# Kernel optimization log

Hardware: AMD Instinct MI355X
Metric: run time of the kernel (lower is better)

## Reference

```python
import jax, jax.numpy as jnp
import numpy as np
import math

B, P, PIX, D, C = 128, 256, 256, 512, 10
MAX_STEPS, TOL, EPS = 4, 1e-3, 1e-5


def setup_inputs() -> dict:
    key = jax.random.key(0)
    ks = jax.random.split(key, 12)
    pi = math.pi
    return {
        "x": jax.random.normal(ks[0], (B, P, PIX), jnp.float32),
        "Wp": jax.random.normal(ks[1], (D, PIX), jnp.float32) * (1.0 / math.sqrt(PIX)),
        "bp": jnp.zeros((D,), jnp.float32),
        "q_rot": jax.random.uniform(ks[2], (D,), jnp.float32, -pi, pi),
        "k_rot": jax.random.uniform(ks[3], (D,), jnp.float32, -pi, pi),
        "v_rot": jax.random.uniform(ks[4], (D,), jnp.float32, -pi, pi),
        "ff_real": jax.random.normal(ks[5], (D, D), jnp.float32) * (1.0 / math.sqrt(D)),
        "ff_imag": jax.random.uniform(ks[6], (D, D), jnp.float32, -0.01, 0.01),
        "Wr": jax.random.normal(ks[7], (C, D), jnp.float32) * 0.05,
        "br": jnp.zeros((C,), jnp.float32),
        "Wi": jax.random.normal(ks[8], (C, D), jnp.float32) * 0.05,
        "bi": jnp.zeros((C,), jnp.float32),
    }


def _complex_norm(x):
    # normalize magnitude stats over last dim, preserve phase (torch.std uses ddof=1)
    mag = jnp.abs(x)
    mean_mag = jnp.mean(mag, axis=-1, keepdims=True)
    std_mag = jnp.std(mag, axis=-1, keepdims=True, ddof=1)
    norm_mag = (mag - mean_mag) / (std_mag + EPS)
    scale = jnp.tanh(norm_mag) / (mag + EPS)
    return x * scale


def _fro(z):
    return jnp.sqrt(jnp.sum(jnp.abs(z) ** 2))


def _pos_phase():
    pos = jnp.arange(P, dtype=jnp.float32)[:, None]
    dim = jnp.arange(D, dtype=jnp.float32)[None, :]
    freq = 1.0 / (10000.0 ** (dim / D))
    return pos * freq * math.pi  # (P, D)


def reference(x, Wp, bp, q_rot, k_rot, v_rot, ff_real, ff_imag, Wr, br, Wi, bi):
    mag = jnp.tanh(jnp.einsum('bpi,di->bpd', x, Wp) + bp)
    state = mag.astype(jnp.complex64) * jnp.exp(1j * _pos_phase())[None]  # (B,P,D)
    ff = (ff_real + 1j * ff_imag).astype(jnp.complex64)
    eq, ek, ev = jnp.exp(1j * q_rot), jnp.exp(1j * k_rot), jnp.exp(1j * v_rot)
    scale = 8.0 / math.sqrt(D)
    active = jnp.array(True)
    for _ in range(MAX_STEPS):  # fixed small iteration count; updates frozen after convergence
        prev = state
        q, k, v = state * eq, state * ek, state * ev
        interference = jnp.einsum('bpd,bqd->bpq', q, jnp.conj(k))
        attn = jax.nn.softmax(interference.real * scale, axis=-1)
        attn_out = jnp.einsum('bpq,bqd->bpd', attn.astype(jnp.complex64), v)
        new_state = _complex_norm((prev + attn_out) @ ff)
        diff = _fro(new_state - prev) / (_fro(new_state) + 1e-8)
        state = jnp.where(active, new_state, prev)
        active = jnp.logical_and(active, diff >= TOL)
    pooled = jnp.mean(state, axis=1)  # (B,D) complex
    logits = pooled.real @ Wr.T + br + pooled.imag @ Wi.T + bi
    return logits
```

## Files before the change

kernel.cpp:

```cpp
#include <hip/hip_runtime.h>
#include <math.h>

#define BB   128
#define PP   256
#define PIX_ 256
#define DD   512
#define CC   10
#define MTOT (BB*PP)
#define NK   1024
#define KA   2048
#define KB2  2048
#define NSLOT (MTOT/4)

static constexpr float SCALE_F = 0.35355339059327373f;
static constexpr float PI_F    = 3.14159265358979323846f;

typedef short bf16x8 __attribute__((ext_vector_type(8)));
typedef float f32x4  __attribute__((ext_vector_type(4)));

__device__ __forceinline__ unsigned short f2bf(float f) {
    union { float f; unsigned u; } v; v.f = f;
    unsigned r = v.u + 0x7FFF + ((v.u >> 16) & 1);
    return (unsigned short)(r >> 16);
}
__device__ __forceinline__ float bf2f(unsigned short h) {
    union { unsigned u; float f; } v; v.u = ((unsigned)h) << 16;
    return v.f;
}

typedef __attribute__((address_space(3))) unsigned lds_u32;
typedef __attribute__((address_space(1))) const unsigned glb_u32;
__device__ __forceinline__ void gl2lds16(const unsigned short* g, short* l) {
    __builtin_amdgcn_global_load_lds((glb_u32*)g, (lds_u32*)l, 16, 0, 0);
}

__global__ void k_setup(const float* __restrict__ q_rot, const float* __restrict__ k_rot,
                        const float* __restrict__ v_rot,
                        float* __restrict__ freq, float* __restrict__ cd, float* __restrict__ sd,
                        float* __restrict__ cv, float* __restrict__ sv,
                        int* __restrict__ active) {
    int t = threadIdx.x;
    if (t < DD) {
        freq[t] = expf(-(float)t * (9.210340371976184f / 512.0f));
        float dl = q_rot[t] - k_rot[t];
        cd[t] = cosf(dl);       sd[t] = sinf(dl);
        cv[t] = cosf(v_rot[t]); sv[t] = sinf(v_rot[t]);
    }
    if (t == 0) *active = 1;
}

__global__ __launch_bounds__(256) void k_prep2(const float* __restrict__ Fr, const float* __restrict__ Fi,
                                               unsigned short* __restrict__ Bt2) {
    const int n = blockIdx.x;
    const int t = threadIdx.x;
    unsigned short* row = Bt2 + (size_t)n * KB2;
#pragma unroll
    for (int j4 = 0; j4 < 4; j4++) {
        const int j = j4 * 256 + t;
        float v;
        if (n < 512) v = (j < 512) ? Fr[(size_t)j * DD + n] : -Fi[(size_t)(j - 512) * DD + n];
        else         v = (j < 512) ? Fi[(size_t)j * DD + (n - 512)] : Fr[(size_t)(j - 512) * DD + (n - 512)];
        const unsigned short hi = f2bf(v);
        row[j] = hi;
        row[NK + j] = f2bf(v - bf2f(hi));
    }
}

__global__ __launch_bounds__(256) void k_packx(const float* __restrict__ x, unsigned short* __restrict__ Xp) {
    const int r = blockIdx.x, t = threadIdx.x;
    const float v = x[(size_t)r * PIX_ + t];
    const unsigned short h = f2bf(v);
    Xp[(size_t)r * 512 + t] = h;
    Xp[(size_t)r * 512 + 256 + t] = f2bf(v - bf2f(h));
}

__global__ __launch_bounds__(256) void k_wpack(const float* __restrict__ Wp, unsigned short* __restrict__ Wt) {
    const int d = blockIdx.x, t = threadIdx.x;
    const float v = Wp[(size_t)d * PIX_ + t];
    const unsigned short h = f2bf(v);
    Wt[(size_t)d * 512 + t] = h;
    Wt[(size_t)d * 512 + 256 + t] = f2bf(v - bf2f(h));
}

#define SCAT4(TILE, V4) do { TILE[lk+0][lrow]=(V4).x; TILE[lk+1][lrow]=(V4).y; \
                             TILE[lk+2][lrow]=(V4).z; TILE[lk+3][lrow]=(V4).w; } while(0)

__global__ __launch_bounds__(256) void k_init(const float* __restrict__ x,
        const float* __restrict__ Wp, const float* __restrict__ bp,
        const float* __restrict__ freq,
        float* __restrict__ Sr, float* __restrict__ Si) {
    __shared__ float As[16][68];
    __shared__ float Bs[16][68];
    const int bm = blockIdx.y * 64, bn = blockIdx.x * 64;
    const int t = threadIdx.x, tx = t & 15, ty = t >> 4;
    const int lrow = t >> 2, lk = (t & 3) * 4;
    float acc[4][4] = {};
    for (int k0 = 0; k0 < PIX_; k0 += 16) {
        const float4 a4 = *(const float4*)(x  + (size_t)(bm + lrow) * PIX_ + k0 + lk);
        const float4 b4 = *(const float4*)(Wp + (size_t)(bn + lrow) * PIX_ + k0 + lk);
        __syncthreads();
        SCAT4(As, a4);
        SCAT4(Bs, b4);
        __syncthreads();
#pragma unroll
        for (int kk = 0; kk < 16; ++kk) {
            const float4 av = *(const float4*)&As[kk][ty * 4];
            const float4 bv = *(const float4*)&Bs[kk][tx * 4];
            const float a[4] = {av.x, av.y, av.z, av.w};
            const float b[4] = {bv.x, bv.y, bv.z, bv.w};
#pragma unroll
            for (int i = 0; i < 4; i++)
#pragma unroll
                for (int j = 0; j < 4; j++) acc[i][j] = fmaf(a[i], b[j], acc[i][j]);
        }
    }
#pragma unroll
    for (int i = 0; i < 4; i++) {
        const int m = bm + ty * 4 + i;
        const int p = m & 255;
        float4 vr, vi;
        float* pvr = (float*)&vr; float* pvi = (float*)&vi;
#pragma unroll
        for (int j = 0; j < 4; j++) {
            const int d = bn + tx * 4 + j;
            const float mg = tanhf(acc[i][j] + bp[d]);
            const float ph = (float)p * freq[d] * PI_F;
            float sph, cph; sincosf(ph, &sph, &cph);
            pvr[j] = mg * cph; pvi[j] = mg * sph;
        }
        *(float4*)(Sr + (size_t)m * DD + bn + tx * 4) = vr;
        *(float4*)(Si + (size_t)m * DD + bn + tx * 4) = vi;
    }
}

__global__ __launch_bounds__(256) void k_init_mfma(const unsigned short* __restrict__ Xp,
        const unsigned short* __restrict__ Wt, const float* __restrict__ bp,
        const float* __restrict__ freq,
        float* __restrict__ Sr, float* __restrict__ Si) {
    __shared__ short AH[128][32], AL[128][32];
    __shared__ short BH[128][32], BL[128][32];
    const int t = threadIdx.x, w = t >> 6, L = t & 63;
    const int lane15 = L & 15, quad = L >> 4;
    const int bm = blockIdx.y * 128, bn = blockIdx.x * 128;
    const int gr = t >> 2, ch = (t & 3) * 8;
    short* AHw = &AH[0][0] + w * 512;
    short* ALw = &AL[0][0] + w * 512;
    short* BHw = &BH[0][0] + w * 512;
    short* BLw = &BL[0][0] + w * 512;
    f32x4 acc[2][8] = {};
    for (int k0 = 0; k0 < 256; k0 += 32) {
        __syncthreads();
        gl2lds16(Xp + (size_t)(bm + gr) * 512      + k0 + ch,       AHw);
        gl2lds16(Xp + (size_t)(bm + 64 + gr) * 512 + k0 + ch,       AHw + 64 * 32);
        gl2lds16(Xp + (size_t)(bm + gr) * 512      + 256 + k0 + ch, ALw);
        gl2lds16(Xp + (size_t)(bm + 64 + gr) * 512 + 256 + k0 + ch, ALw + 64 * 32);
        gl2lds16(Wt + (size_t)(bn + gr) * 512      + k0 + ch,       BHw);
        gl2lds16(Wt + (size_t)(bn + 64 + gr) * 512 + k0 + ch,       BHw + 64 * 32);
        gl2lds16(Wt + (size_t)(bn + gr) * 512      + 256 + k0 + ch, BLw);
        gl2lds16(Wt + (size_t)(bn + 64 + gr) * 512 + 256 + k0 + ch, BLw + 64 * 32);
        __syncthreads();
        bf16x8 ah[2], al[2];
#pragma unroll
        for (int tr = 0; tr < 2; tr++) {
            ah[tr] = *(const bf16x8*)&AH[w * 32 + tr * 16 + lane15][quad * 8];
            al[tr] = *(const bf16x8*)&AL[w * 32 + tr * 16 + lane15][quad * 8];
        }
#pragma unroll
        for (int tc = 0; tc < 8; tc++) {
            const bf16x8 bh = *(const bf16x8*)&BH[tc * 16 + lane15][quad * 8];
            acc[0][tc] = __builtin_amdgcn_mfma_f32_16x16x32_bf16(ah[0], bh, acc[0][tc], 0, 0, 0);
            acc[1][tc] = __builtin_amdgcn_mfma_f32_16x16x32_bf16(ah[1], bh, acc[1][tc], 0, 0, 0);
            acc[0][tc] = __builtin_amdgcn_mfma_f32_16x16x32_bf16(al[0], bh, acc[0][tc], 0, 0, 0);
            acc[1][tc] = __builtin_amdgcn_mfma_f32_16x16x32_bf16(al[1], bh, acc[1][tc], 0, 0, 0);
            const bf16x8 bl = *(const bf16x8*)&BL[tc * 16 + lane15][quad * 8];
            acc[0][tc] = __builtin_amdgcn_mfma_f32_16x16x32_bf16(ah[0], bl, acc[0][tc], 0, 0, 0);
            acc[1][tc] = __builtin_amdgcn_mfma_f32_16x16x32_bf16(ah[1], bl, acc[1][tc], 0, 0, 0);
        }
    }
#pragma unroll
    for (int tr = 0; tr < 2; tr++)
#pragma unroll
        for (int tc = 0; tc < 8; tc++) {
            const int d = bn + tc * 16 + lane15;
            const float bpd = bp[d];
            const float fq = freq[d] * PI_F;
#pragma unroll
            for (int r = 0; r < 4; r++) {
                const int m = bm + w * 32 + tr * 16 + quad * 4 + r;
                const int p = m & 255;
                const float mg = tanhf(acc[tr][tc][r] + bpd);
                float sph, cph; sincosf((float)p * fq, &sph, &cph);
                Sr[(size_t)m * DD + d] = mg * cph;
                Si[(size_t)m * DD + d] = mg * sph;
            }
        }
}

__global__ __launch_bounds__(256) void k_xy(const float* __restrict__ Sr, const float* __restrict__ Si,
        const float* __restrict__ cd, const float* __restrict__ sd,
        unsigned short* X, unsigned short* Y,
        const int* __restrict__ active) {
    if (*active == 0) return;
    const int r = blockIdx.x, t = threadIdx.x;
    const size_t base = (size_t)r * DD + 2 * t;
    const float2 s_r = *(const float2*)(Sr + base);
    const float2 s_i = *(const float2*)(Si + base);
    const float2 c2  = *(const float2*)(cd + 2 * t);
    const float2 s2  = *(const float2*)(sd + 2 * t);
    unsigned short* xr = X + (size_t)r * KA;
    unsigned short* yr = Y + (size_t)r * KA;
    const float srv[2] = {s_r.x, s_r.y}, siv[2] = {s_i.x, s_i.y};
    const float cv_[2] = {c2.x, c2.y},  sv_[2] = {s2.x, s2.y};
    ushort2 xh_r, xh_i, xl_r, xl_i, yh_r, yh_i, yl_r, yl_i;
    unsigned short* o[8] = {(unsigned short*)&xh_r, (unsigned short*)&xh_i,
                            (unsigned short*)&xl_r, (unsigned short*)&xl_i,
                            (unsigned short*)&yh_r, (unsigned short*)&yh_i,
                            (unsigned short*)&yl_r, (unsigned short*)&yl_i};
#pragma unroll
    for (int e = 0; e < 2; e++) {
        const unsigned short hr = f2bf(srv[e]);
        const unsigned short hi_ = f2bf(siv[e]);
        o[0][e] = hr;  o[2][e] = f2bf(srv[e] - bf2f(hr));
        o[1][e] = hi_; o[3][e] = f2bf(siv[e] - bf2f(hi_));
        const float krr = srv[e] * cv_[e] + siv[e] * sv_[e];
        const float kri = siv[e] * cv_[e] - srv[e] * sv_[e];
        const unsigned short yh1 = f2bf(krr);
        const unsigned short yh2 = f2bf(kri);
        o[4][e] = yh1; o[6][e] = f2bf(krr - bf2f(yh1));
        o[5][e] = yh2; o[7][e] = f2bf(kri - bf2f(yh2));
    }
    *(ushort2*)(xr + 2 * t)        = xh_r;
    *(ushort2*)(xr + 512 + 2 * t)  = xh_i;
    *(ushort2*)(xr + 1024 + 2 * t) = xl_r;
    *(ushort2*)(xr + 1536 + 2 * t) = xl_i;
    *(ushort2*)(yr + 2 * t)        = yh_r;
    *(ushort2*)(yr + 512 + 2 * t)  = yh_i;
    *(ushort2*)(yr + 1024 + 2 * t) = yl_r;
    *(ushort2*)(yr + 1536 + 2 * t) = yl_i;
}

__global__ __launch_bounds__(256) void k_score_sm(const unsigned short* __restrict__ X,
        const unsigned short* __restrict__ Y,
        unsigned short* __restrict__ Asp, const int* __restrict__ active) {
    if (*active == 0) return;
    __shared__ short XH[64][32], XL[64][32];
    __shared__ short YH[256][32], YL[256][32];
    const int t = threadIdx.x;
    const int w = t >> 6, L = t & 63;
    const int lane15 = L & 15, quad = L >> 4;
    const int bm = blockIdx.x * 64;
    const int yb = ((int)blockIdx.x >> 2) * 256;
    const int gr = t >> 2, ch = (t & 3) * 8;
    short* XHw = &XH[0][0] + w * 512;
    short* XLw = &XL[0][0] + w * 512;
    short* YHw = &YH[0][0] + w * 512;
    short* YLw = &YL[0][0] + w * 512;
    f32x4 acc[16] = {};
    for (int k0 = 0; k0 < 1024; k0 += 32) {
        __syncthreads();
        gl2lds16(X + (size_t)(bm + gr) * KA + k0 + ch,        XHw);
        gl2lds16(X + (size_t)(bm + gr) * KA + 1024 + k0 + ch, XLw);
#pragma unroll
        for (int s = 0; s < 4; s++) {
            gl2lds16(Y + (size_t)(yb + s * 64 + gr) * KA + k0 + ch,        YHw + s * 2048);
            gl2lds16(Y + (size_t)(yb + s * 64 + gr) * KA + 1024 + k0 + ch, YLw + s * 2048);
        }
        __syncthreads();
        const bf16x8 xh = *(const bf16x8*)&XH[w * 16 + lane15][quad * 8];
        const bf16x8 xl = *(const bf16x8*)&XL[w * 16 + lane15][quad * 8];
#pragma unroll
        for (int tc = 0; tc < 16; tc++) {
            const bf16x8 yh = *(const bf16x8*)&YH[tc * 16 + lane15][quad * 8];
            acc[tc] = __builtin_amdgcn_mfma_f32_16x16x32_bf16(xh, yh, acc[tc], 0, 0, 0);
            acc[tc] = __builtin_amdgcn_mfma_f32_16x16x32_bf16(xl, yh, acc[tc], 0, 0, 0);
            const bf16x8 yl = *(const bf16x8*)&YL[tc * 16 + lane15][quad * 8];
            acc[tc] = __builtin_amdgcn_mfma_f32_16x16x32_bf16(xh, yl, acc[tc], 0, 0, 0);
        }
    }
#pragma unroll
    for (int tc = 0; tc < 16; tc++) acc[tc] *= SCALE_F;
#pragma unroll
    for (int r = 0; r < 4; r++) {
        float mx = acc[0][r];
#pragma unroll
        for (int tc = 1; tc < 16; tc++) mx = fmaxf(mx, acc[tc][r]);
#pragma unroll
        for (int off = 8; off; off >>= 1) mx = fmaxf(mx, __shfl_xor(mx, off, 64));
        float s = 0.f;
        float e[16];
#pragma unroll
        for (int tc = 0; tc < 16; tc++) { e[tc] = __expf(acc[tc][r] - mx); s += e[tc]; }
#pragma unroll
        for (int off = 8; off; off >>= 1) s += __shfl_xor(s, off, 64);
        const float inv = 1.0f / s;
        const int row = bm + w * 16 + quad * 4 + r;
        unsigned short* o = Asp + (size_t)row * 512;
#pragma unroll
        for (int tc = 0; tc < 16; tc++) {
            const float p = e[tc] * inv;
            const unsigned short h = f2bf(p);
            o[tc * 16 + lane15] = h;
            o[256 + tc * 16 + lane15] = f2bf(p - bf2f(h));
        }
    }
}

__global__ __launch_bounds__(256) void k_attnout_mfma(const unsigned short* __restrict__ Asp,
        const unsigned short* __restrict__ X,
        const float* __restrict__ Sr, const float* __restrict__ Si,
        const float* __restrict__ cv, const float* __restrict__ sv,
        unsigned short* __restrict__ A2, const int* __restrict__ active) {
    if (*active == 0) return;
    __shared__ short AhT[128][32];
    __shared__ short AlT[128][32];
    __shared__ short BH[128][40];
    __shared__ short BL[128][40];
    const int t = threadIdx.x;
    const int w = t >> 6, L = t & 63;
    const int lane15 = L & 15, quad = L >> 4;
    const int bm = blockIdx.y * 128;
    const int bn = blockIdx.x * 64;
    const int sample = blockIdx.y >> 1;
    const int gr = t >> 2, ch = (t & 3) * 8;
    short* AhW0 = &AhT[0][0] + w * 512;
    short* AhW1 = AhW0 + 64 * 32;
    short* AlW0 = &AlT[0][0] + w * 512;
    short* AlW1 = AlW0 + 64 * 32;
    const int nn = t & 127, kh = t >> 7;
    const unsigned short* Bsrc = X + (size_t)sample * PP * KA
                               + ((nn < 64) ? (bn + nn) : (512 + bn + nn - 64));
    f32x4 acc[2][8] = {};
    for (int q0 = 0; q0 < PP; q0 += 32) {
        __syncthreads();
        gl2lds16(Asp + (size_t)(bm + gr) * 512      + q0 + ch,       AhW0);
        gl2lds16(Asp + (size_t)(bm + 64 + gr) * 512 + q0 + ch,       AhW1);
        gl2lds16(Asp + (size_t)(bm + gr) * 512      + 256 + q0 + ch, AlW0);
        gl2lds16(Asp + (size_t)(bm + 64 + gr) * 512 + 256 + q0 + ch, AlW1);
#pragma unroll
        for (int kg = 0; kg < 2; kg++) {
            const int qb = kh * 16 + kg * 8;
            bf16x8 hh, ll;
#pragma unroll
            for (int j = 0; j < 8; j++) {
                const size_t o = (size_t)(q0 + qb + j) * KA;
                hh[j] = (short)Bsrc[o];
                ll[j] = (short)Bsrc[o + 1024];
            }
            *(bf16x8*)&BH[nn][qb] = hh;
            *(bf16x8*)&BL[nn][qb] = ll;
        }
        __syncthreads();
        bf16x8 bh[8];
#pragma unroll
        for (int tc = 0; tc < 8; tc++)
            bh[tc] = *(const bf16x8*)&BH[tc * 16 + lane15][quad * 8];
        bf16x8 afh[2];
#pragma unroll
        for (int tr = 0; tr < 2; tr++) {
            afh[tr] = *(const bf16x8*)&AhT[w * 32 + tr * 16 + lane15][quad * 8];
            const bf16x8 afl = *(const bf16x8*)&AlT[w * 32 + tr * 16 + lane15][quad * 8];
#pragma unroll
            for (int tc = 0; tc < 8; tc++)
                acc[tr][tc] = __builtin_amdgcn_mfma_f32_16x16x32_bf16(afh[tr], bh[tc], acc[tr][tc], 0, 0, 0);
#pragma unroll
            for (int tc = 0; tc < 8; tc++)
                acc[tr][tc] = __builtin_amdgcn_mfma_f32_16x16x32_bf16(afl, bh[tc], acc[tr][tc], 0, 0, 0);
        }
#pragma unroll
        for (int tc = 0; tc < 8; tc++) {
            const bf16x8 bl = *(const bf16x8*)&BL[tc * 16 + lane15][quad * 8];
            acc[0][tc] = __builtin_amdgcn_mfma_f32_16x16x32_bf16(afh[0], bl, acc[0][tc], 0, 0, 0);
            acc[1][tc] = __builtin_amdgcn_mfma_f32_16x16x32_bf16(afh[1], bl, acc[1][tc], 0, 0, 0);
        }
    }
#pragma unroll
    for (int tr = 0; tr < 2; tr++) {
#pragma unroll
        for (int tc = 0; tc < 4; tc++) {
            const int d = bn + tc * 16 + lane15;
            const float cvd = cv[d], svd = sv[d];
#pragma unroll
            for (int r = 0; r < 4; r++) {
                const int m = bm + w * 32 + tr * 16 + quad * 4 + r;
                const float wr = acc[tr][tc][r];
                const float wi = acc[tr][tc + 4][r];
                const float tr_ = Sr[(size_t)m * DD + d] + (wr * cvd - wi * svd);
                const float ti_ = Si[(size_t)m * DD + d] + (wr * svd + wi * cvd);
                const unsigned short rh = f2bf(tr_);
                const unsigned short ih = f2bf(ti_);
                unsigned short* arow = A2 + (size_t)m * KA;
                arow[d]        = rh;
                arow[512 + d]  = ih;
                arow[1024 + d] = f2bf(tr_ - bf2f(rh));
                arow[1536 + d] = f2bf(ti_ - bf2f(ih));
            }
        }
    }
}

__global__ __launch_bounds__(256) void k_ff_mfma2(const unsigned short* __restrict__ A2,
        const unsigned short* __restrict__ Bt2,
        float* __restrict__ U, const int* __restrict__ active) {
    if (*active == 0) return;
    __shared__ short AH[128][32], AL[128][32];
    __shared__ short BH[128][32], BL[128][32];
    const int t = threadIdx.x;
    const int w = t >> 6, L = t & 63;
    const int lane15 = L & 15, quad = L >> 4;
    const int bm = blockIdx.y * 128, bn = blockIdx.x * 128;
    const int gr = t >> 2, ch = (t & 3) * 8;
    short* AHw = &AH[0][0] + w * 512;
    short* ALw = &AL[0][0] + w * 512;
    short* BHw = &BH[0][0] + w * 512;
    short* BLw = &BL[0][0] + w * 512;
    f32x4 acc[2][8] = {};
    for (int k0 = 0; k0 < 1024; k0 += 32) {
        __syncthreads();
        gl2lds16(A2  + (size_t)(bm + gr) * KA       + k0 + ch,        AHw);
        gl2lds16(A2  + (size_t)(bm + 64 + gr) * KA  + k0 + ch,        AHw + 64 * 32);
        gl2lds16(A2  + (size_t)(bm + gr) * KA       + 1024 + k0 + ch, ALw);
        gl2lds16(A2  + (size_t)(bm + 64 + gr) * KA  + 1024 + k0 + ch, ALw + 64 * 32);
        gl2lds16(Bt2 + (size_t)(bn + gr) * KB2      + k0 + ch,        BHw);
        gl2lds16(Bt2 + (size_t)(bn + 64 + gr) * KB2 + k0 + ch,        BHw + 64 * 32);
        gl2lds16(Bt2 + (size_t)(bn + gr) * KB2      + 1024 + k0 + ch, BLw);
        gl2lds16(Bt2 + (size_t)(bn + 64 + gr) * KB2 + 1024 + k0 + ch, BLw + 64 * 32);
        __syncthreads();
        bf16x8 ah[2], al[2];
#pragma unroll
        for (int tr = 0; tr < 2; tr++) {
            ah[tr] = *(const bf16x8*)&AH[w * 32 + tr * 16 + lane15][quad * 8];
            al[tr] = *(const bf16x8*)&AL[w * 32 + tr * 16 + lane15][quad * 8];
        }
#pragma unroll
        for (int tc = 0; tc < 8; tc++) {
            const bf16x8 bh = *(const bf16x8*)&BH[tc * 16 + lane15][quad * 8];
            acc[0][tc] = __builtin_amdgcn_mfma_f32_16x16x32_bf16(ah[0], bh, acc[0][tc], 0, 0, 0);
            acc[1][tc] = __builtin_amdgcn_mfma_f32_16x16x32_bf16(ah[1], bh, acc[1][tc], 0, 0, 0);
            acc[0][tc] = __builtin_amdgcn_mfma_f32_16x16x32_bf16(al[0], bh, acc[0][tc], 0, 0, 0);
            acc[1][tc] = __builtin_amdgcn_mfma_f32_16x16x32_bf16(al[1], bh, acc[1][tc], 0, 0, 0);
            const bf16x8 bl = *(const bf16x8*)&BL[tc * 16 + lane15][quad * 8];
            acc[0][tc] = __builtin_amdgcn_mfma_f32_16x16x32_bf16(ah[0], bl, acc[0][tc], 0, 0, 0);
            acc[1][tc] = __builtin_amdgcn_mfma_f32_16x16x32_bf16(ah[1], bl, acc[1][tc], 0, 0, 0);
        }
    }
#pragma unroll
    for (int tr = 0; tr < 2; tr++)
#pragma unroll
        for (int tc = 0; tc < 8; tc++) {
            const int n = bn + tc * 16 + lane15;
            const int mbase = bm + w * 32 + tr * 16 + quad * 4;
#pragma unroll
            for (int r = 0; r < 4; r++)
                U[(size_t)(mbase + r) * NK + n] = acc[tr][tc][r];
        }
}

__global__ __launch_bounds__(256) void k_norm(const float* U,
        float* __restrict__ Sr, float* __restrict__ Si,
        float* __restrict__ part,
        unsigned short* X, unsigned short* Y,
        const float* __restrict__ cd, const float* __restrict__ sd,
        const int wxy, const int* __restrict__ active) {
    if (*active == 0) return;
    __shared__ float red[8];
    const int t = threadIdx.x, rt = t >> 6, L = t & 63;
    const int row = blockIdx.x * 4 + rt;
    const size_t ub = (size_t)row * NK;
    const size_t base = (size_t)row * DD;
    const float4 ur0 = *(const float4*)(U + ub + 4 * L);
    const float4 ur1 = *(const float4*)(U + ub + 256 + 4 * L);
    const float4 ui0 = *(const float4*)(U + ub + 512 + 4 * L);
    const float4 ui1 = *(const float4*)(U + ub + 768 + 4 * L);
    const float4 pr0 = *(const float4*)(Sr + base + 4 * L);
    const float4 pr1 = *(const float4*)(Sr + base + 256 + 4 * L);
    const float4 pi0 = *(const float4*)(Si + base + 4 * L);
    const float4 pi1 = *(const float4*)(Si + base + 256 + 4 * L);
    const float urr[8] = {ur0.x, ur0.y, ur0.z, ur0.w, ur1.x, ur1.y, ur1.z, ur1.w};
    const float uii[8] = {ui0.x, ui0.y, ui0.z, ui0.w, ui1.x, ui1.y, ui1.z, ui1.w};
    float mg[8], msum = 0.f;
#pragma unroll
    for (int e = 0; e < 8; e++) {
        mg[e] = sqrtf(urr[e] * urr[e] + uii[e] * uii[e]);
        msum += mg[e];
    }
#pragma unroll
    for (int off = 32; off; off >>= 1) msum += __shfl_xor(msum, off, 64);
    const float mean = msum * (1.0f / 512.0f);
    float vs = 0.f;
#pragma unroll
    for (int e = 0; e < 8; e++) { const float d = mg[e] - mean; vs += d * d; }
#pragma unroll
    for (int off = 32; off; off >>= 1) vs += __shfl_xor(vs, off, 64);
    const float istd = 1.0f / (sqrtf(vs * (1.0f / 511.0f)) + 1e-5f);
    float nr[8], ni[8];
#pragma unroll
    for (int e = 0; e < 8; e++) {
        const float sc = tanhf((mg[e] - mean) * istd) / (mg[e] + 1e-5f);
        nr[e] = urr[e] * sc; ni[e] = uii[e] * sc;
    }
    const float prr[8] = {pr0.x, pr0.y, pr0.z, pr0.w, pr1.x, pr1.y, pr1.z, pr1.w};
    const float pii[8] = {pi0.x, pi0.y, pi0.z, pi0.w, pi1.x, pi1.y, pi1.z, pi1.w};
    float dd = 0.f, nn = 0.f;
#pragma unroll
    for (int e = 0; e < 8; e++) {
        const float dr = nr[e] - prr[e], di = ni[e] - pii[e];
        dd += dr * dr + di * di;
        nn += nr[e] * nr[e] + ni[e] * ni[e];
    }
    *(float4*)(Sr + base + 4 * L)       = make_float4(nr[0], nr[1], nr[2], nr[3]);
    *(float4*)(Sr + base + 256 + 4 * L) = make_float4(nr[4], nr[5], nr[6], nr[7]);
    *(float4*)(Si + base + 4 * L)       = make_float4(ni[0], ni[1], ni[2], ni[3]);
    *(float4*)(Si + base + 256 + 4 * L) = make_float4(ni[4], ni[5], ni[6], ni[7]);
    if (wxy) {
        unsigned short* xr = X + (size_t)row * KA;
        unsigned short* yr = Y + (size_t)row * KA;
        const float4 c0 = *(const float4*)(cd + 4 * L);
        const float4 c1 = *(const float4*)(cd + 256 + 4 * L);
        const float4 s0 = *(const float4*)(sd + 4 * L);
        const float4 s1 = *(const float4*)(sd + 256 + 4 * L);
        const float cdv[8] = {c0.x, c0.y, c0.z, c0.w, c1.x, c1.y, c1.z, c1.w};
        const float sdv[8] = {s0.x, s0.y, s0.z, s0.w, s1.x, s1.y, s1.z, s1.w};
        ushort4 xhr[2], xhi[2], xlr[2], xli[2], yhr[2], yhi[2], ylr[2], yli[2];
#pragma unroll
        for (int e = 0; e < 8; e++) {
            const int g = e >> 2, j = e & 3;
            const unsigned short hr = f2bf(nr[e]);
            const unsigned short hi_ = f2bf(ni[e]);
            ((unsigned short*)&xhr[g])[j] = hr;
            ((unsigned short*)&xlr[g])[j] = f2bf(nr[e] - bf2f(hr));
            ((unsigned short*)&xhi[g])[j] = hi_;
            ((unsigned short*)&xli[g])[j] = f2bf(ni[e] - bf2f(hi_));
            const float krr = nr[e] * cdv[e] + ni[e] * sdv[e];
            const float kri = ni[e] * cdv[e] - nr[e] * sdv[e];
            const unsigned short k1 = f2bf(krr);
            const unsigned short k2 = f2bf(kri);
            ((unsigned short*)&yhr[g])[j] = k1;
            ((unsigned short*)&ylr[g])[j] = f2bf(krr - bf2f(k1));
            ((unsigned short*)&yhi[g])[j] = k2;
            ((unsigned short*)&yli[g])[j] = f2bf(kri - bf2f(k2));
        }
        *(ushort4*)(xr + 4 * L)        = xhr[0]; *(ushort4*)(xr + 256 + 4 * L)  = xhr[1];
        *(ushort4*)(xr + 512 + 4 * L)  = xhi[0]; *(ushort4*)(xr + 768 + 4 * L)  = xhi[1];
        *(ushort4*)(xr + 1024 + 4 * L) = xlr[0]; *(ushort4*)(xr + 1280 + 4 * L) = xlr[1];
        *(ushort4*)(xr + 1536 + 4 * L) = xli[0]; *(ushort4*)(xr + 1792 + 4 * L) = xli[1];
        *(ushort4*)(yr + 4 * L)        = yhr[0]; *(ushort4*)(yr + 256 + 4 * L)  = yhr[1];
        *(ushort4*)(yr + 512 + 4 * L)  = yhi[0]; *(ushort4*)(yr + 768 + 4 * L)  = yhi[1];
        *(ushort4*)(yr + 1024 + 4 * L) = ylr[0]; *(ushort4*)(yr + 1280 + 4 * L) = ylr[1];
        *(ushort4*)(yr + 1536 + 4 * L) = yli[0]; *(ushort4*)(yr + 1792 + 4 * L) = yli[1];
    }
#pragma unroll
    for (int off = 32; off; off >>= 1) {
        dd += __shfl_xor(dd, off, 64);
        nn += __shfl_xor(nn, off, 64);
    }
    if (L == 0) { red[rt] = dd; red[4 + rt] = nn; }
    __syncthreads();
    if (t == 0)
        *(float2*)(part + 2 * blockIdx.x) =
            make_float2(red[0] + red[1] + red[2] + red[3],
                        red[4] + red[5] + red[6] + red[7]);
}

__global__ __launch_bounds__(256) void k_flag(const float* __restrict__ part, int* __restrict__ active) {
    __shared__ float red[8];
    const int t = threadIdx.x, rt = t >> 6, L = t & 63;
    float dd = 0.f, nn = 0.f;
    for (int i = t; i < NSLOT; i += 256) {
        const float2 p = *(const float2*)(part + 2 * i);
        dd += p.x; nn += p.y;
    }
#pragma unroll
    for (int off = 32; off; off >>= 1) {
        dd += __shfl_xor(dd, off, 64);
        nn += __shfl_xor(nn, off, 64);
    }
    if (L == 0) { red[rt] = dd; red[4 + rt] = nn; }
    __syncthreads();
    if (t == 0) {
        const float d = red[0] + red[1] + red[2] + red[3];
        const float n = red[4] + red[5] + red[6] + red[7];
        const float diff = sqrtf(d) / (sqrtf(n) + 1e-8f);
        const int a = *active;
        *active = (a && (diff >= 1e-3f)) ? 1 : 0;
    }
}

__global__ __launch_bounds__(256) void k_pool(const float* __restrict__ Sr, const float* __restrict__ Si,
        float* __restrict__ Pr, float* __restrict__ Pi) {
    const int gid = blockIdx.x * 256 + threadIdx.x;
    const int b = gid >> 9, d = gid & 511;
    const size_t base = (size_t)b * PP * DD + d;
    float sr = 0.f, si = 0.f;
    for (int p = 0; p < PP; p++) {
        sr += Sr[base + (size_t)p * DD];
        si += Si[base + (size_t)p * DD];
    }
    Pr[gid] = sr * (1.0f / 256.0f);
    Pi[gid] = si * (1.0f / 256.0f);
}

__global__ __launch_bounds__(64) void k_logits(const float* __restrict__ Pr, const float* __restrict__ Pi,
        const float* __restrict__ Wr, const float* __restrict__ br,
        const float* __restrict__ Wi, const float* __restrict__ bi,
        float* __restrict__ out) {
    const int b = blockIdx.x;
    const int lane = threadIdx.x;
    for (int c = 0; c < CC; c++) {
        float acc = 0.f;
#pragma unroll
        for (int k = 0; k < 8; k++) {
            const int d = lane + 64 * k;
            acc += Pr[b * DD + d] * Wr[c * DD + d] + Pi[b * DD + d] * Wi[c * DD + d];
        }
#pragma unroll
        for (int off = 32; off; off >>= 1) acc += __shfl_xor(acc, off, 64);
        if (lane == 0) out[b * CC + c] = acc + br[c] + bi[c];
    }
}

extern "C" void kernel_launch(void* const* d_in, const int* in_sizes, int n_in,
                              void* d_out, int out_size, void* d_ws, size_t ws_size,
                              hipStream_t stream) {
    const float* x     = (const float*)d_in[0];
    const float* Wp    = (const float*)d_in[1];
    const float* bp    = (const float*)d_in[2];
    const float* q_rot = (const float*)d_in[3];
    const float* k_rot = (const float*)d_in[4];
    const float* v_rot = (const float*)d_in[5];
    const float* ffr   = (const float*)d_in[6];
    const float* ffi   = (const float*)d_in[7];
    const float* Wr    = (const float*)d_in[8];
    const float* br    = (const float*)d_in[9];
    const float* Wi    = (const float*)d_in[10];
    const float* bi    = (const float*)d_in[11];
    float* out = (float*)d_out;

    float* ws = (float*)d_ws;
    const size_t plane = (size_t)MTOT * DD;
    const size_t sline = (size_t)PP * DD;

    float* freq = ws;
    float* cd   = freq + DD;
    float* sd   = cd + DD;
    float* cv   = sd + DD;
    float* sv   = cv + DD;
    int*   active = (int*)(sv + DD);
    float* Pr = ws + 4096;
    float* Pi = Pr + (size_t)BB * DD;
    float* part = Pi + (size_t)BB * DD;
    float* Sr = part + 2 * NSLOT;
    float* Si = Sr + plane;
    unsigned short* Bt2 = (unsigned short*)(Si + plane);
    unsigned short* Wt  = Bt2 + (size_t)NK * KB2;
    float* chunkbase = Si + plane + (size_t)NK * 3072 / 2;

    const size_t fixed_f = (4096 + 2 * (size_t)BB * DD + 2 * NSLOT) + 2 * plane + (size_t)NK * 3072 / 2;
    const size_t perC_f = (size_t)PP * NK * 2 + (size_t)PP * 256;

    int C = BB;
    while (C > 1 && (fixed_f + (size_t)C * perC_f) * 4ull > ws_size) C >>= 1;
    const int fullXY = (C == BB);
    const int mfmaInit = (C >= 32);

    float* U = chunkbase;
    unsigned short* X  = (unsigned short*)chunkbase;
    float* Yf = chunkbase + (size_t)C * PP * NK;
    unsigned short* Y  = (unsigned short*)Yf;
    unsigned short* A2 = Y;
    unsigned short* Asp = (unsigned short*)(Yf + (size_t)C * PP * NK);
    unsigned short* Xp = (unsigned short*)chunkbase;

    k_setup<<<1, 512, 0, stream>>>(q_rot, k_rot, v_rot, freq, cd, sd, cv, sv, active);
    k_prep2<<<NK, 256, 0, stream>>>(ffr, ffi, Bt2);
    if (mfmaInit) {
        k_packx<<<MTOT, 256, 0, stream>>>(x, Xp);
        k_wpack<<<DD, 256, 0, stream>>>(Wp, Wt);
        k_init_mfma<<<dim3(DD / 128, MTOT / 128), 256, 0, stream>>>(Xp, Wt, bp, freq, Sr, Si);
    } else {
        k_init<<<dim3(DD / 64, MTOT / 64), 256, 0, stream>>>(x, Wp, bp, freq, Sr, Si);
    }

    for (int it = 0; it < 4; ++it) {
        for (int c0 = 0; c0 < BB; c0 += C) {
            float* Sr_c = Sr + (size_t)c0 * sline;
            float* Si_c = Si + (size_t)c0 * sline;
            float* part_c = part + (size_t)c0 * (PP / 4) * 2;
            if (!fullXY || it == 0)
                k_xy<<<C * PP, 256, 0, stream>>>(Sr_c, Si_c, cd, sd, X, Y, active);
            k_score_sm<<<C * 4, 256, 0, stream>>>(X, Y, Asp, active);
            k_attnout_mfma<<<dim3(8, C * 2), 256, 0, stream>>>(Asp, X, Sr_c, Si_c, cv, sv, A2, active);
            k_ff_mfma2<<<dim3(NK / 128, C * 2), 256, 0, stream>>>(A2, Bt2, U, active);
            k_norm<<<C * (PP / 4), 256, 0, stream>>>(U, Sr_c, Si_c, part_c, X, Y, cd, sd, fullXY, active);
        }
        k_flag<<<1, 256, 0, stream>>>(part, active);
    }

    k_pool<<<BB * DD / 256, 256, 0, stream>>>(Sr, Si, Pr, Pi);
    k_logits<<<BB, 64, 0, stream>>>(Pr, Pi, Wr, br, Wi, bi, out);
}
```

Baseline: 3.268 ms.

## Reorder block grids so M tiles vary fastest and stage init epilogue through LDS

Swaps the grid dimensions of the init, attention-output and FF GEMMs so consecutive workgroups walk along M while sharing the same N tile. The score kernel's block index is remapped to interleave samples, which changes which blocks run concurrently and so cache locality and spread across XCDs. The init GEMM epilogue now writes results into LDS tiles and emits coalesced float4 global stores instead of scattered scalar stores. The extra 68 KB of shared memory in init lowers its occupancy, and the grid reordering may lose B-tile reuse in L2.

```diff
diff --git a/kernel.cpp b/kernel.cpp
--- a/kernel.cpp
+++ b/kernel.cpp
@@ -139,9 +139,11 @@
         float* __restrict__ Sr, float* __restrict__ Si) {
     __shared__ short AH[128][32], AL[128][32];
     __shared__ short BH[128][32], BL[128][32];
+    __shared__ float TBr[128][68];
+    __shared__ float TBi[128][68];
     const int t = threadIdx.x, w = t >> 6, L = t & 63;
     const int lane15 = L & 15, quad = L >> 4;
-    const int bm = blockIdx.y * 128, bn = blockIdx.x * 128;
+    const int bm = blockIdx.x * 128, bn = blockIdx.y * 128;
     const int gr = t >> 2, ch = (t & 3) * 8;
     short* AHw = &AH[0][0] + w * 512;
     short* ALw = &AL[0][0] + w * 512;
@@ -178,22 +180,37 @@
         }
     }
 #pragma unroll
-    for (int tr = 0; tr < 2; tr++)
-#pragma unroll
-        for (int tc = 0; tc < 8; tc++) {
-            const int d = bn + tc * 16 + lane15;
-            const float bpd = bp[d];
-            const float fq = freq[d] * PI_F;
-#pragma unroll
-            for (int r = 0; r < 4; r++) {
-                const int m = bm + w * 32 + tr * 16 + quad * 4 + r;
-                const int p = m & 255;
-                const float mg = tanhf(acc[tr][tc][r] + bpd);
-                float sph, cph; sincosf((float)p * fq, &sph, &cph);
-                Sr[(size_t)m * DD + d] = mg * cph;
-                Si[(size_t)m * DD + d] = mg * sph;
+    for (int h = 0; h < 2; h++) {
+        __syncthreads();
+#pragma unroll
+        for (int tr = 0; tr < 2; tr++)
+#pragma unroll
+            for (int tc = 0; tc < 4; tc++) {
+                const int tcg = h * 4 + tc;
+                const int d = bn + tcg * 16 + lane15;
+                const float bpd = bp[d];
+                const float fq = freq[d] * PI_F;
+#pragma unroll
+                for (int r = 0; r < 4; r++) {
+                    const int m = w * 32 + tr * 16 + quad * 4 + r;
+                    const int p = (bm + m) & 255;
+                    const float mg = tanhf(acc[tr][tcg][r] + bpd);
+                    float sph, cph; sincosf((float)p * fq, &sph, &cph);
+                    TBr[m][tc * 16 + lane15] = mg * cph;
+                    TBi[m][tc * 16 + lane15] = mg * sph;
+                }
             }
-        }
+        __syncthreads();
+#pragma unroll
+        for (int g = 0; g < 8; g++) {
+            const int row = (t >> 4) + g * 16;
+            const int col = (t & 15) * 4;
+            const float4 vr = *(const float4*)&TBr[row][col];
+            const float4 vi = *(const float4*)&TBi[row][col];
+            *(float4*)(Sr + (size_t)(bm + row) * DD + bn + h * 64 + col) = vr;
+            *(float4*)(Si + (size_t)(bm + row) * DD + bn + h * 64 + col) = vi;
+        }
+    }
 }
 
 __global__ __launch_bounds__(256) void k_xy(const float* __restrict__ Sr, const float* __restrict__ Si,
@@ -248,8 +265,11 @@
     const int t = threadIdx.x;
     const int w = t >> 6, L = t & 63;
     const int lane15 = L & 15, quad = L >> 4;
-    const int bm = blockIdx.x * 64;
-    const int yb = ((int)blockIdx.x >> 2) * 256;
+    const int nsm = (int)gridDim.x >> 2;
+    const int s   = (int)blockIdx.x & (nsm - 1);
+    const int rt  = (int)blockIdx.x / nsm;
+    const int bm = s * 256 + rt * 64;
+    const int yb = s * 256;
     const int gr = t >> 2, ch = (t & 3) * 8;
     short* XHw = &XH[0][0] + w * 512;
     short* XLw = &XL[0][0] + w * 512;
@@ -261,9 +281,9 @@
         gl2lds16(X + (size_t)(bm + gr) * KA + k0 + ch,        XHw);
         gl2lds16(X + (size_t)(bm + gr) * KA + 1024 + k0 + ch, XLw);
 #pragma unroll
-        for (int s = 0; s < 4; s++) {
-            gl2lds16(Y + (size_t)(yb + s * 64 + gr) * KA + k0 + ch,        YHw + s * 2048);
-            gl2lds16(Y + (size_t)(yb + s * 64 + gr) * KA + 1024 + k0 + ch, YLw + s * 2048);
+        for (int ss = 0; ss < 4; ss++) {
+            gl2lds16(Y + (size_t)(yb + ss * 64 + gr) * KA + k0 + ch,        YHw + ss * 2048);
+            gl2lds16(Y + (size_t)(yb + ss * 64 + gr) * KA + 1024 + k0 + ch, YLw + ss * 2048);
         }
         __syncthreads();
         const bf16x8 xh = *(const bf16x8*)&XH[w * 16 + lane15][quad * 8];
@@ -286,13 +306,13 @@
         for (int tc = 1; tc < 16; tc++) mx = fmaxf(mx, acc[tc][r]);
 #pragma unroll
         for (int off = 8; off; off >>= 1) mx = fmaxf(mx, __shfl_xor(mx, off, 64));
-        float s = 0.f;
+        float sum = 0.f;
         float e[16];
 #pragma unroll
-        for (int tc = 0; tc < 16; tc++) { e[tc] = __expf(acc[tc][r] - mx); s += e[tc]; }
-#pragma unroll
-        for (int off = 8; off; off >>= 1) s += __shfl_xor(s, off, 64);
-        const float inv = 1.0f / s;
+        for (int tc = 0; tc < 16; tc++) { e[tc] = __expf(acc[tc][r] - mx); sum += e[tc]; }
+#pragma unroll
+        for (int off = 8; off; off >>= 1) sum += __shfl_xor(sum, off, 64);
+        const float inv = 1.0f / sum;
         const int row = bm + w * 16 + quad * 4 + r;
         unsigned short* o = Asp + (size_t)row * 512;
 #pragma unroll
@@ -318,9 +338,9 @@
     const int t = threadIdx.x;
     const int w = t >> 6, L = t & 63;
     const int lane15 = L & 15, quad = L >> 4;
-    const int bm = blockIdx.y * 128;
-    const int bn = blockIdx.x * 64;
-    const int sample = blockIdx.y >> 1;
+    const int bm = blockIdx.x * 128;
+    const int bn = blockIdx.y * 64;
+    const int sample = blockIdx.x >> 1;
     const int gr = t >> 2, ch = (t & 3) * 8;
     short* AhW0 = &AhT[0][0] + w * 512;
     short* AhW1 = AhW0 + 64 * 32;
@@ -407,7 +427,7 @@
     const int t = threadIdx.x;
     const int w = t >> 6, L = t & 63;
     const int lane15 = L & 15, quad = L >> 4;
-    const int bm = blockIdx.y * 128, bn = blockIdx.x * 128;
+    const int bm = blockIdx.x * 128, bn = blockIdx.y * 128;
     const int gr = t >> 2, ch = (t & 3) * 8;
     short* AHw = &AH[0][0] + w * 512;
     short* ALw = &AL[0][0] + w * 512;
@@ -675,7 +695,7 @@
     if (mfmaInit) {
         k_packx<<<MTOT, 256, 0, stream>>>(x, Xp);
         k_wpack<<<DD, 256, 0, stream>>>(Wp, Wt);
-        k_init_mfma<<<dim3(DD / 128, MTOT / 128), 256, 0, stream>>>(Xp, Wt, bp, freq, Sr, Si);
+        k_init_mfma<<<dim3(MTOT / 128, DD / 128), 256, 0, stream>>>(Xp, Wt, bp, freq, Sr, Si);
     } else {
         k_init<<<dim3(DD / 64, MTOT / 64), 256, 0, stream>>>(x, Wp, bp, freq, Sr, Si);
     }
@@ -688,8 +708,8 @@
             if (!fullXY || it == 0)
                 k_xy<<<C * PP, 256, 0, stream>>>(Sr_c, Si_c, cd, sd, X, Y, active);
             k_score_sm<<<C * 4, 256, 0, stream>>>(X, Y, Asp, active);
-            k_attnout_mfma<<<dim3(8, C * 2), 256, 0, stream>>>(Asp, X, Sr_c, Si_c, cv, sv, A2, active);
-            k_ff_mfma2<<<dim3(NK / 128, C * 2), 256, 0, stream>>>(A2, Bt2, U, active);
+            k_attnout_mfma<<<dim3(C * 2, 8), 256, 0, stream>>>(Asp, X, Sr_c, Si_c, cv, sv, A2, active);
+            k_ff_mfma2<<<dim3(C * 2, NK / 128), 256, 0, stream>>>(A2, Bt2, U, active);
             k_norm<<<C * (PP / 4), 256, 0, stream>>>(U, Sr_c, Si_c, part_c, X, Y, cd, sd, fullXY, active);
         }
         k_flag<<<1, 256, 0, stream>>>(part, active);
```

After: 3.124 ms. -4.4%, faster.
